# Kernel tuning notes

Measured on AMD Instinct MI355X. Metric: run time of the kernel, lower is better.

The kernel has to match this reference:

```python
import jax, jax.numpy as jnp
import numpy as np

N = 50000      # nodes
E = 800000     # edges (avg degree 16)
LM = 1024      # lm_dim
H = 128        # hidden_channels
OUT = 64       # out_channels


def setup_inputs() -> dict:
    key = jax.random.key(0)
    ks = jax.random.split(key, 13)
    s = 0.02
    return {
        "x": jax.random.normal(ks[0], (N,), dtype=jnp.float32),
        "x_out": jax.random.normal(ks[1], (N, LM), dtype=jnp.float32),
        "c": jax.random.normal(ks[2], (N,), dtype=jnp.float32),
        "edge_index": jax.random.randint(ks[3], (2, E), 0, N, dtype=jnp.int64),
        "edge_weight": jax.random.uniform(ks[4], (E,), dtype=jnp.float32),
        # weights stored as [in, out]
        "Wa": jax.random.normal(ks[5], (1, LM), dtype=jnp.float32) * s,   # aa_linear (no bias)
        "Wc": jax.random.normal(ks[6], (1, LM), dtype=jnp.float32) * s,   # c_linear (no bias)
        "Wl": jax.random.normal(ks[7], (LM, LM), dtype=jnp.float32) * s,  # lm_linear
        "bl": jax.random.normal(ks[8], (LM,), dtype=jnp.float32) * s,
        "W1": jax.random.normal(ks[9], (LM, H), dtype=jnp.float32) * s,   # conv1
        "b1": jax.random.normal(ks[10], (H,), dtype=jnp.float32) * s,
        "W3": jax.random.normal(ks[11], (H, OUT), dtype=jnp.float32) * s,  # conv3
        "b3": jax.random.normal(ks[12], (OUT,), dtype=jnp.float32) * s,
    }


def gcn_conv(h, src, dst, ew, W, b, n):
    """PyG GCNConv with normalize=True, add_self_loops=True."""
    h = h @ W                                   # [n, out]
    loop = jnp.arange(n, dtype=src.dtype)
    src_f = jnp.concatenate([src, loop])
    dst_f = jnp.concatenate([dst, loop])
    ew_f = jnp.concatenate([ew, jnp.ones((n,), ew.dtype)])
    deg = jax.ops.segment_sum(ew_f, dst_f, num_segments=n)     # in-degree incl. self-loops
    dis = jnp.where(deg > 0, jax.lax.rsqrt(deg), 0.0)          # deg^{-1/2}
    norm = dis[src_f] * ew_f * dis[dst_f]                      # per-edge coefficient
    out = jax.ops.segment_sum(norm[:, None] * h[src_f], dst_f, num_segments=n)
    return out + b


def reference(x, x_out, c, edge_index, edge_weight, Wa, Wc, Wl, bl, W1, b1, W3, b3):
    # (c_linear(c[:,None]) + aa_linear(x[:,None]) + lm_linear(x_out)).relu()
    h = jax.nn.relu(c[:, None] * Wc[0] + x[:, None] * Wa[0] + x_out @ Wl + bl)  # [N, LM]
    src, dst = edge_index[0], edge_index[1]
    h = jax.nn.relu(gcn_conv(h, src, dst, edge_weight, W1, b1, N))              # [N, H]
    return gcn_conv(h, src, dst, edge_weight, W3, b3, N)                        # [N, OUT]
```

## Files before the change

### kernel.cpp

```cpp
#include <hip/hip_runtime.h>
#include <hip/hip_bf16.h>

typedef unsigned short u16;
typedef unsigned long long u64;
typedef __attribute__((ext_vector_type(8))) short bf16x8;
typedef __attribute__((ext_vector_type(4))) float f32x4;

constexpr int NN = 50000;
constexpr int NE = 800000;
constexpr int LM = 1024;
constexpr int HC = 128;
constexpr int OC = 64;

constexpr size_t OFF_ROWPTR = 0;
constexpr size_t OFF_CURSOR = 200192;
constexpr size_t OFF_PK     = 400384;
constexpr size_t OFF_INCL   = 800512;
constexpr size_t OFF_BSUM   = 1000704;
constexpr size_t OFF_DIS    = 1000960;
constexpr size_t OFF_META   = 1201152;
constexpr size_t OFF_WLT    = 7601408;
constexpr size_t OFF_W1T    = 9698560;
constexpr size_t OFF_H      = 9960704;
constexpr size_t OFF_Y1     = 112360704;
constexpr size_t OFF_Y3     = 125160704;
constexpr size_t OFF_ABF    = 131560704;
constexpr size_t NEED_FAST  = OFF_ABF + (size_t)NN * LM * 2;

__device__ __forceinline__ u16 f2bf(float f) {
    union { float f; unsigned int u; } a; a.f = f;
    unsigned int u = a.u + 0x7FFFu + ((a.u >> 16) & 1u);
    return (u16)(u >> 16);
}
__device__ __forceinline__ float bf2f(u16 v) {
    union { unsigned int u; float f; } a; a.u = ((unsigned int)v) << 16;
    return a.f;
}
__device__ __forceinline__ ushort2 pkbf(float a, float b) {
    union { __hip_bfloat162 h; ushort2 u; } cv;
    cv.h = __float22bfloat162_rn(make_float2(a, b));
    return cv.u;
}
__device__ __forceinline__ void async_copy16(u16* lds, const u16* g) {
    __builtin_amdgcn_global_load_lds(
        (const __attribute__((address_space(1))) void*)g,
        (__attribute__((address_space(3))) void*)lds, 16, 0, 0);
}

__global__ void k_setup(u64* __restrict__ pk,
                        const float* __restrict__ Wl, u16* __restrict__ WlT,
                        const float* __restrict__ W1, u16* __restrict__ W1T,
                        const float* __restrict__ A32, u16* __restrict__ Abf) {
    int b = blockIdx.x, t = threadIdx.x;
    if (b >= 1732) {
        size_t idx = (size_t)(b - 1732) * 256 + t;
        const float* src = A32 + idx * 8;
        float4 v0 = *(const float4*)(src);
        float4 v1 = *(const float4*)(src + 4);
        union { ushort2 u2[4]; bf16x8 v; } pk2;
        pk2.u2[0] = pkbf(v0.x, v0.y);
        pk2.u2[1] = pkbf(v0.z, v0.w);
        pk2.u2[2] = pkbf(v1.x, v1.y);
        pk2.u2[3] = pkbf(v1.z, v1.w);
        *(bf16x8*)(Abf + idx * 8) = pk2.v;
    } else if (b < 196) {
        int i = b * 256 + t;
        if (i < NN) pk[i] = 0ULL;
    } else if (b < 196 + 1024) {
        __shared__ float sm[32][33];
        int bb = b - 196;
        int n0 = (bb & 31) * 32, k0 = (bb >> 5) * 32;
        int ty = t >> 5, tx = t & 31;
        #pragma unroll
        for (int i = 0; i < 4; i++)
            sm[ty + i * 8][tx] = Wl[(size_t)(k0 + ty + i * 8) * LM + n0 + tx];
        __syncthreads();
        #pragma unroll
        for (int i = 0; i < 4; i++)
            WlT[(size_t)(n0 + ty + i * 8) * LM + k0 + tx] = f2bf(sm[tx][ty + i * 8]);
    } else {
        int idx = (b - 1220) * 256 + t;
        if (idx < HC * LM) {
            int o = idx >> 10, k = idx & 1023;
            W1T[idx] = f2bf(W1[(size_t)k * HC + o]);
        }
    }
}

__global__ void k_count(const int* __restrict__ ei, const float* __restrict__ ew,
                        u64* __restrict__ pk) {
    int e = blockIdx.x * 256 + threadIdx.x;
    if (e < NE) {
        int d = ei[NE + e];
        u64 add = (1ULL << 48) | (u64)(ew[e] * 4294967296.0);
        atomicAdd(&pk[d], add);
    }
}
__global__ void k_scan1(const u64* __restrict__ pk, int* __restrict__ incl,
                        int* __restrict__ bsum) {
    __shared__ int sm[1024];
    int t = threadIdx.x, idx = blockIdx.x * 1024 + t;
    int v = (idx < NN) ? (int)(pk[idx] >> 48) : 0;
    sm[t] = v; __syncthreads();
    for (int off = 1; off < 1024; off <<= 1) {
        int add = (t >= off) ? sm[t - off] : 0;
        __syncthreads();
        sm[t] += add;
        __syncthreads();
    }
    if (idx < NN) incl[idx] = sm[t];
    if (t == 1023) bsum[blockIdx.x] = sm[t];
}
__global__ void k_scan3(const int* __restrict__ incl, const u64* __restrict__ pk,
                        const int* __restrict__ bsum,
                        int* __restrict__ rowptr, int* __restrict__ cursor,
                        float* __restrict__ dis) {
    int seg = blockIdx.x >> 2;
    int lane = threadIdx.x & 63;
    int v = (lane < seg) ? bsum[lane] : 0;
    #pragma unroll
    for (int off = 32; off > 0; off >>= 1) v += __shfl_down(v, off, 64);
    int boffv = __shfl(v, 0, 64);
    int idx = blockIdx.x * 256 + threadIdx.x;
    if (idx < NN) {
        u64 p = pk[idx];
        int cnt = (int)(p >> 48);
        float deg = (float)((double)(p & 0xFFFFFFFFFFFFULL) * 2.3283064365386963e-10);
        int rp = incl[idx] - cnt + boffv;
        rowptr[idx] = rp;
        cursor[idx] = rp;
        dis[idx] = rsqrtf(1.0f + deg);
    } else if (idx == NN) {
        rowptr[NN] = NE;
    }
}
__global__ void k_fill(const int* __restrict__ ei, const float* __restrict__ ew,
                       const float* __restrict__ dis,
                       int* __restrict__ cursor, int2* __restrict__ meta) {
    int e = blockIdx.x * 256 + threadIdx.x;
    if (e < NE) {
        int s = ei[e];
        int d = ei[NE + e];
        int slot = atomicAdd(&cursor[d], 1);
        meta[slot] = make_int2(s, __float_as_int(ew[e] * dis[s]));
    }
}

__global__ __launch_bounds__(256, 4) void k_gemm1a(
    const u16* __restrict__ Abf, const u16* __restrict__ Bt, u16* __restrict__ Cout,
    const float* __restrict__ xv, const float* __restrict__ cv,
    const float* __restrict__ Wa, const float* __restrict__ Wc,
    const float* __restrict__ bl) {
    __shared__ u16 lA[128 * 64];
    __shared__ u16 lB[128 * 64];
    const int tid = threadIdx.x;
    const int lane = tid & 63, wv = tid >> 6;
    int x = blockIdx.x & 7, j = blockIdx.x >> 3;
    int bx = (j & ~7) | x;
    int by = j & 7;
    if (bx >= 391) return;
    const int m0 = bx * 128, n0 = by * 128;
    const int wm = (wv >> 1) * 64, wn = (wv & 1) * 64;
    const int fr = lane & 15, qd = lane >> 4;

    f32x4 acc[4][4] = {};

    for (int kt = 0; kt < 16; kt++) {
        const int k0 = kt << 6;
        __syncthreads();
        #pragma unroll
        for (int i = 0; i < 4; i++) {
            int r0 = i * 32 + wv * 8;
            int rl = r0 + (lane >> 3);
            int slot = lane & 7;
            int k8 = slot ^ (rl & 7);
            const u16* g = Bt + (size_t)(n0 + rl) * LM + k0 + k8 * 8;
            async_copy16(&lB[r0 * 64], g);
        }
        #pragma unroll
        for (int i = 0; i < 4; i++) {
            int r0 = i * 32 + wv * 8;
            int rl = r0 + (lane >> 3);
            int slot = lane & 7;
            int k8 = slot ^ (rl & 7);
            int row = m0 + rl; if (row >= NN) row = NN - 1;
            const u16* g = Abf + (size_t)row * LM + k0 + k8 * 8;
            async_copy16(&lA[r0 * 64], g);
        }
        __syncthreads();
        #pragma unroll
        for (int s = 0; s < 2; s++) {
            const int slot = (s * 4 + qd) ^ (fr & 7);
            bf16x8 af[4], bfm[4];
            #pragma unroll
            for (int mi = 0; mi < 4; mi++)
                af[mi] = *(const bf16x8*)&lA[(wm + mi * 16 + fr) * 64 + slot * 8];
            #pragma unroll
            for (int ni = 0; ni < 4; ni++)
                bfm[ni] = *(const bf16x8*)&lB[(wn + ni * 16 + fr) * 64 + slot * 8];
            #pragma unroll
            for (int mi = 0; mi < 4; mi++)
                #pragma unroll
                for (int ni = 0; ni < 4; ni++)
                    acc[mi][ni] = __builtin_amdgcn_mfma_f32_16x16x32_bf16(
                        af[mi], bfm[ni], acc[mi][ni], 0, 0, 0);
        }
    }

    int jj[4]; float waj[4], wcj[4], blj[4];
    #pragma unroll
    for (int ni = 0; ni < 4; ni++) {
        jj[ni] = n0 + wn + ni * 16 + fr;
        waj[ni] = Wa[jj[ni]]; wcj[ni] = Wc[jj[ni]]; blj[ni] = bl[jj[ni]];
    }
    #pragma unroll
    for (int mi = 0; mi < 4; mi++)
        #pragma unroll
        for (int r = 0; r < 4; r++) {
            int row = m0 + wm + mi * 16 + qd * 4 + r;
            if (row < NN) {
                float xb = xv[row], cb = cv[row];
                #pragma unroll
                for (int ni = 0; ni < 4; ni++) {
                    float v = acc[mi][ni][r] + xb * waj[ni] + cb * wcj[ni] + blj[ni];
                    Cout[(size_t)row * LM + jj[ni]] = f2bf(fmaxf(v, 0.f));
                }
            }
        }
}

__global__ __launch_bounds__(256, 2) void k_gemm1f(
    const float* __restrict__ A32, const u16* __restrict__ Bt, u16* __restrict__ Cout,
    const float* __restrict__ xv, const float* __restrict__ cv,
    const float* __restrict__ Wa, const float* __restrict__ Wc,
    const float* __restrict__ bl) {
    __shared__ u16 lA[128 * 64];
    __shared__ u16 lB[2][128 * 64];
    const int tid = threadIdx.x;
    const int lane = tid & 63, wv = tid >> 6;
    const int bx = ((blockIdx.x >> 5) << 3) | (blockIdx.x & 7);
    const int by = (blockIdx.x >> 3) & 3;
    if (bx >= 391) return;
    const int m0 = bx * 128, n0 = by * 256;
    const int wm = (wv >> 1) * 64, wn = (wv & 1) * 64;
    const int fr = lane & 15, qd = lane >> 4;

    f32x4 acc[2][4][4] = {};

    int srl[4], sslot[4]; const float* sbase[4];
    float4 pf[8];
    #pragma unroll
    for (int i = 0; i < 4; i++) {
        int cidx = i * 256 + tid;
        srl[i] = cidx >> 3; sslot[i] = cidx & 7;
        int k8 = sslot[i] ^ (srl[i] & 7);
        int row = m0 + srl[i]; if (row >= NN) row = NN - 1;
        sbase[i] = A32 + (size_t)row * LM + k8 * 8;
    }
    #pragma unroll
    for (int i = 0; i < 4; i++) {
        pf[2 * i]     = *(const float4*)(sbase[i]);
        pf[2 * i + 1] = *(const float4*)(sbase[i] + 4);
    }

    for (int kt = 0; kt < 16; kt++) {
        const int k0 = kt << 6;
        __syncthreads();
        #pragma unroll
        for (int h = 0; h < 2; h++)
            #pragma unroll
            for (int i = 0; i < 4; i++) {
                int r0 = i * 32 + wv * 8;
                int rl = r0 + (lane >> 3);
                int slot = lane & 7;
                int k8 = slot ^ (rl & 7);
                const u16* g = Bt + (size_t)(n0 + h * 128 + rl) * LM + k0 + k8 * 8;
                async_copy16(&lB[h][r0 * 64], g);
            }
        #pragma unroll
        for (int i = 0; i < 4; i++) {
            union { ushort2 u2[4]; bf16x8 v; } pk;
            pk.u2[0] = pkbf(pf[2 * i].x, pf[2 * i].y);
            pk.u2[1] = pkbf(pf[2 * i].z, pf[2 * i].w);
            pk.u2[2] = pkbf(pf[2 * i + 1].x, pf[2 * i + 1].y);
            pk.u2[3] = pkbf(pf[2 * i + 1].z, pf[2 * i + 1].w);
            *(bf16x8*)&lA[srl[i] * 64 + sslot[i] * 8] = pk.v;
        }
        __syncthreads();
        if (kt < 15) {
            #pragma unroll
            for (int i = 0; i < 4; i++) {
                pf[2 * i]     = *(const float4*)(sbase[i] + k0 + 64);
                pf[2 * i + 1] = *(const float4*)(sbase[i] + k0 + 68);
            }
        }
        #pragma unroll
        for (int s = 0; s < 2; s++) {
            const int slot = (s * 4 + qd) ^ (fr & 7);
            bf16x8 af[4];
            #pragma unroll
            for (int mi = 0; mi < 4; mi++)
                af[mi] = *(const bf16x8*)&lA[(wm + mi * 16 + fr) * 64 + slot * 8];
            #pragma unroll
            for (int h = 0; h < 2; h++) {
                bf16x8 bfm[4];
                #pragma unroll
                for (int ni = 0; ni < 4; ni++)
                    bfm[ni] = *(const bf16x8*)&lB[h][(wn + ni * 16 + fr) * 64 + slot * 8];
                #pragma unroll
                for (int mi = 0; mi < 4; mi++)
                    #pragma unroll
                    for (int ni = 0; ni < 4; ni++)
                        acc[h][mi][ni] = __builtin_amdgcn_mfma_f32_16x16x32_bf16(
                            af[mi], bfm[ni], acc[h][mi][ni], 0, 0, 0);
            }
        }
    }

    #pragma unroll
    for (int h = 0; h < 2; h++) {
        int jj[4]; float waj[4], wcj[4], blj[4];
        #pragma unroll
        for (int ni = 0; ni < 4; ni++) {
            jj[ni] = n0 + h * 128 + wn + ni * 16 + fr;
            waj[ni] = Wa[jj[ni]]; wcj[ni] = Wc[jj[ni]]; blj[ni] = bl[jj[ni]];
        }
        #pragma unroll
        for (int mi = 0; mi < 4; mi++)
            #pragma unroll
            for (int r = 0; r < 4; r++) {
                int row = m0 + wm + mi * 16 + qd * 4 + r;
                if (row < NN) {
                    float xb = xv[row], cb = cv[row];
                    #pragma unroll
                    for (int ni = 0; ni < 4; ni++) {
                        float v = acc[h][mi][ni][r] + xb * waj[ni] + cb * wcj[ni] + blj[ni];
                        Cout[(size_t)row * LM + jj[ni]] = f2bf(fmaxf(v, 0.f));
                    }
                }
            }
    }
}

__global__ __launch_bounds__(256) void k_gemm2(
    const u16* __restrict__ Abf, const u16* __restrict__ Bt, u16* __restrict__ Cout) {
    __shared__ u16 lA[64 * 64];
    __shared__ u16 lB[128 * 64];
    const int tid = threadIdx.x;
    const int lane = tid & 63, wv = tid >> 6;
    const int m0 = blockIdx.x * 64;
    const int wm = (wv >> 1) * 32, wn = (wv & 1) * 64;
    const int fr = lane & 15, qd = lane >> 4;
    f32x4 acc[2][4] = {};

    for (int kt = 0; kt < 16; kt++) {
        const int k0 = kt << 6;
        __syncthreads();
        #pragma unroll
        for (int i = 0; i < 4; i++) {
            int r0 = i * 32 + wv * 8;
            int rl = r0 + (lane >> 3);
            int slot = lane & 7;
            int k8 = slot ^ (rl & 7);
            const u16* g = Bt + (size_t)rl * LM + k0 + k8 * 8;
            async_copy16(&lB[r0 * 64], g);
        }
        #pragma unroll
        for (int i = 0; i < 2; i++) {
            int r0 = i * 32 + wv * 8;
            int rl = r0 + (lane >> 3);
            int slot = lane & 7;
            int k8 = slot ^ (rl & 7);
            int row = m0 + rl; if (row >= NN) row = NN - 1;
            const u16* g = Abf + (size_t)row * LM + k0 + k8 * 8;
            async_copy16(&lA[r0 * 64], g);
        }
        __syncthreads();
        #pragma unroll
        for (int s = 0; s < 2; s++) {
            const int slot = (s * 4 + qd) ^ (fr & 7);
            bf16x8 af[2], bfm[4];
            #pragma unroll
            for (int mi = 0; mi < 2; mi++)
                af[mi] = *(const bf16x8*)&lA[(wm + mi * 16 + fr) * 64 + slot * 8];
            #pragma unroll
            for (int ni = 0; ni < 4; ni++)
                bfm[ni] = *(const bf16x8*)&lB[(wn + ni * 16 + fr) * 64 + slot * 8];
            #pragma unroll
            for (int mi = 0; mi < 2; mi++)
                #pragma unroll
                for (int ni = 0; ni < 4; ni++)
                    acc[mi][ni] = __builtin_amdgcn_mfma_f32_16x16x32_bf16(
                        af[mi], bfm[ni], acc[mi][ni], 0, 0, 0);
        }
    }
    #pragma unroll
    for (int mi = 0; mi < 2; mi++)
        #pragma unroll
        for (int r = 0; r < 4; r++) {
            int row = m0 + wm + mi * 16 + qd * 4 + r;
            if (row < NN) {
                #pragma unroll
                for (int ni = 0; ni < 4; ni++)
                    Cout[(size_t)row * HC + wn + ni * 16 + fr] = f2bf(acc[mi][ni][r]);
            }
        }
}

__global__ __launch_bounds__(512) void k_agg1g3(
    const u16* __restrict__ y1, const int* __restrict__ rowptr,
    const int2* __restrict__ meta, const float* __restrict__ dis,
    const float* __restrict__ b1, const float* __restrict__ W3,
    u16* __restrict__ y3) {
    __shared__ float hrow[8][HC];
    int wv = threadIdx.x >> 6, lane = threadIdx.x & 63;
    int node = blockIdx.x * 8 + wv;
    if (node >= NN) return;
    float di = dis[node];
    int p0 = rowptr[node], p1 = rowptr[node + 1];
    ushort2 sv = *(const ushort2*)(y1 + (size_t)node * HC + lane * 2);
    float a0 = di * bf2f(sv.x), a1 = di * bf2f(sv.y);
    #pragma unroll 8
    for (int p = p0; p < p1; ++p) {
        int2 m = meta[p];
        float nm = __int_as_float(m.y);
        ushort2 v = *(const ushort2*)(y1 + (size_t)m.x * HC + lane * 2);
        a0 += nm * bf2f(v.x);
        a1 += nm * bf2f(v.y);
    }
    a0 = fmaxf(di * a0 + b1[lane * 2], 0.f);
    a1 = fmaxf(di * a1 + b1[lane * 2 + 1], 0.f);
    hrow[wv][lane * 2] = a0;
    hrow[wv][lane * 2 + 1] = a1;
    float acc = 0.f;
    #pragma unroll 8
    for (int k = 0; k < HC; ++k)
        acc += hrow[wv][k] * W3[(size_t)k * OC + lane];
    y3[(size_t)node * OC + lane] = f2bf(acc);
}

__global__ __launch_bounds__(256) void k_agg3(
    const u16* __restrict__ y3, const int* __restrict__ rowptr,
    const int2* __restrict__ meta, const float* __restrict__ dis,
    const float* __restrict__ b3, float* __restrict__ outp) {
    int node = blockIdx.x * 4 + (threadIdx.x >> 6);
    int lane = threadIdx.x & 63;
    if (node >= NN) return;
    float di = dis[node];
    int p0 = rowptr[node], p1 = rowptr[node + 1];
    float a = di * bf2f(y3[(size_t)node * OC + lane]);
    #pragma unroll 8
    for (int p = p0; p < p1; ++p) {
        int2 m = meta[p];
        a += __int_as_float(m.y) * bf2f(y3[(size_t)m.x * OC + lane]);
    }
    outp[(size_t)node * OC + lane] = di * a + b3[lane];
}

extern "C" void kernel_launch(void* const* d_in, const int* in_sizes, int n_in,
                              void* d_out, int out_size, void* d_ws, size_t ws_size,
                              hipStream_t stream) {
    const float* x    = (const float*)d_in[0];
    const float* xout = (const float*)d_in[1];
    const float* c    = (const float*)d_in[2];
    const int*   ei   = (const int*)d_in[3];
    const float* ew   = (const float*)d_in[4];
    const float* Wa   = (const float*)d_in[5];
    const float* Wc   = (const float*)d_in[6];
    const float* Wl   = (const float*)d_in[7];
    const float* bl   = (const float*)d_in[8];
    const float* W1   = (const float*)d_in[9];
    const float* b1   = (const float*)d_in[10];
    const float* W3   = (const float*)d_in[11];
    const float* b3   = (const float*)d_in[12];
    float* outp = (float*)d_out;

    char* ws = (char*)d_ws;
    int*   rowptr = (int*)(ws + OFF_ROWPTR);
    int*   cursor = (int*)(ws + OFF_CURSOR);
    u64*   pk     = (u64*)(ws + OFF_PK);
    int*   incl   = (int*)(ws + OFF_INCL);
    int*   bsum   = (int*)(ws + OFF_BSUM);
    float* dis    = (float*)(ws + OFF_DIS);
    int2*  meta   = (int2*)(ws + OFF_META);
    u16*   WlT    = (u16*)(ws + OFF_WLT);
    u16*   W1T    = (u16*)(ws + OFF_W1T);
    u16*   hbuf   = (u16*)(ws + OFF_H);
    u16*   y1     = (u16*)(ws + OFF_Y1);
    u16*   y3     = (u16*)(ws + OFF_Y3);
    u16*   Abf    = (u16*)(ws + OFF_ABF);

    const bool fast = (ws_size >= NEED_FAST);

    k_setup<<<fast ? 26732 : 1732, 256, 0, stream>>>(pk, Wl, WlT, W1, W1T, xout, Abf);
    k_count<<<3125, 256, 0, stream>>>(ei, ew, pk);
    k_scan1<<<49, 1024, 0, stream>>>(pk, incl, bsum);
    k_scan3<<<196, 256, 0, stream>>>(incl, pk, bsum, rowptr, cursor, dis);
    k_fill <<<3125, 256, 0, stream>>>(ei, ew, dis, cursor, meta);

    if (fast) {
        k_gemm1a<<<392 * 8, 256, 0, stream>>>(Abf, WlT, hbuf, x, c, Wa, Wc, bl);
    } else {
        k_gemm1f<<<49 * 32, 256, 0, stream>>>(xout, WlT, hbuf, x, c, Wa, Wc, bl);
    }
    k_gemm2<<<782, 256, 0, stream>>>(hbuf, W1T, y1);
    k_agg1g3<<<6250, 512, 0, stream>>>(y1, rowptr, meta, dis, b1, W3, y3);
    k_agg3<<<12500, 256, 0, stream>>>(y3, rowptr, meta, dis, b3, outp);
}
```

Measured before the change: 663.7 us.

## Spread x_out bf16 conversion across graph-preprocessing kernels to overlap latency-bound work

```diff
diff --git a/kernel.cpp b/kernel.cpp
--- a/kernel.cpp
+++ b/kernel.cpp
@@ -27,6 +27,12 @@
 constexpr size_t OFF_ABF    = 131560704;
 constexpr size_t NEED_FAST  = OFF_ABF + (size_t)NN * LM * 2;
 
+constexpr size_t CVT_TOTAL = (size_t)NN * LM / 8;
+constexpr size_t CVT_CNT   = 2560000;
+constexpr size_t CVT_SC1   = 1280000;
+constexpr size_t CVT_SC3   = 640000;
+constexpr size_t CVT_FIL   = 1920000;
+
 __device__ __forceinline__ u16 f2bf(float f) {
     union { float f; unsigned int u; } a; a.f = f;
     unsigned int u = a.u + 0x7FFFu + ((a.u >> 16) & 1u);
@@ -46,29 +52,40 @@
         (const __attribute__((address_space(1))) void*)g,
         (__attribute__((address_space(3))) void*)lds, 16, 0, 0);
 }
-
-__global__ void k_setup(u64* __restrict__ pk,
+__device__ __forceinline__ void cvt_chunk(size_t idx, const float* __restrict__ A32,
+                                          u16* __restrict__ Abf) {
+    const float* src = A32 + idx * 8;
+    float4 v0 = *(const float4*)(src);
+    float4 v1 = *(const float4*)(src + 4);
+    union { ushort2 u2[4]; bf16x8 v; } pk2;
+    pk2.u2[0] = pkbf(v0.x, v0.y);
+    pk2.u2[1] = pkbf(v0.z, v0.w);
+    pk2.u2[2] = pkbf(v1.x, v1.y);
+    pk2.u2[3] = pkbf(v1.z, v1.w);
+    *(bf16x8*)(Abf + idx * 8) = pk2.v;
+}
+
+__global__ void k_zero(u64* __restrict__ pk) {
+    int i = blockIdx.x * 256 + threadIdx.x;
+    if (i < NN) pk[i] = 0ULL;
+}
+
+__global__ void k_count(const int* __restrict__ ei, const float* __restrict__ ew,
+                        u64* __restrict__ pk,
                         const float* __restrict__ Wl, u16* __restrict__ WlT,
                         const float* __restrict__ W1, u16* __restrict__ W1T,
                         const float* __restrict__ A32, u16* __restrict__ Abf) {
     int b = blockIdx.x, t = threadIdx.x;
-    if (b >= 1732) {
-        size_t idx = (size_t)(b - 1732) * 256 + t;
-        const float* src = A32 + idx * 8;
-        float4 v0 = *(const float4*)(src);
-        float4 v1 = *(const float4*)(src + 4);
-        union { ushort2 u2[4]; bf16x8 v; } pk2;
-        pk2.u2[0] = pkbf(v0.x, v0.y);
-        pk2.u2[1] = pkbf(v0.z, v0.w);
-        pk2.u2[2] = pkbf(v1.x, v1.y);
-        pk2.u2[3] = pkbf(v1.z, v1.w);
-        *(bf16x8*)(Abf + idx * 8) = pk2.v;
-    } else if (b < 196) {
-        int i = b * 256 + t;
-        if (i < NN) pk[i] = 0ULL;
-    } else if (b < 196 + 1024) {
+    if (b < 3125) {
+        int e = b * 256 + t;
+        if (e < NE) {
+            int d = ei[NE + e];
+            u64 add = (1ULL << 48) | (u64)(ew[e] * 4294967296.0);
+            atomicAdd(&pk[d], add);
+        }
+    } else if (b < 4149) {
         __shared__ float sm[32][33];
-        int bb = b - 196;
+        int bb = b - 3125;
         int n0 = (bb & 31) * 32, k0 = (bb >> 5) * 32;
         int ty = t >> 5, tx = t & 31;
         #pragma unroll
@@ -78,28 +95,27 @@
         #pragma unroll
         for (int i = 0; i < 4; i++)
             WlT[(size_t)(n0 + ty + i * 8) * LM + k0 + tx] = f2bf(sm[tx][ty + i * 8]);
-    } else {
-        int idx = (b - 1220) * 256 + t;
+    } else if (b < 4661) {
+        int idx = (b - 4149) * 256 + t;
         if (idx < HC * LM) {
             int o = idx >> 10, k = idx & 1023;
             W1T[idx] = f2bf(W1[(size_t)k * HC + o]);
         }
-    }
-}
-
-__global__ void k_count(const int* __restrict__ ei, const float* __restrict__ ew,
-                        u64* __restrict__ pk) {
-    int e = blockIdx.x * 256 + threadIdx.x;
-    if (e < NE) {
-        int d = ei[NE + e];
-        u64 add = (1ULL << 48) | (u64)(ew[e] * 4294967296.0);
-        atomicAdd(&pk[d], add);
-    }
-}
+    } else {
+        cvt_chunk((size_t)(b - 4661) * 256 + t, A32, Abf);
+    }
+}
+
 __global__ void k_scan1(const u64* __restrict__ pk, int* __restrict__ incl,
-                        int* __restrict__ bsum) {
+                        int* __restrict__ bsum,
+                        const float* __restrict__ A32, u16* __restrict__ Abf) {
+    int b = blockIdx.x, t = threadIdx.x;
+    if (b >= 49) {
+        cvt_chunk(CVT_CNT + (size_t)(b - 49) * 1024 + t, A32, Abf);
+        return;
+    }
     __shared__ int sm[1024];
-    int t = threadIdx.x, idx = blockIdx.x * 1024 + t;
+    int idx = b * 1024 + t;
     int v = (idx < NN) ? (int)(pk[idx] >> 48) : 0;
     sm[t] = v; __syncthreads();
     for (int off = 1; off < 1024; off <<= 1) {
@@ -109,19 +125,26 @@
         __syncthreads();
     }
     if (idx < NN) incl[idx] = sm[t];
-    if (t == 1023) bsum[blockIdx.x] = sm[t];
-}
+    if (t == 1023) bsum[b] = sm[t];
+}
+
 __global__ void k_scan3(const int* __restrict__ incl, const u64* __restrict__ pk,
                         const int* __restrict__ bsum,
                         int* __restrict__ rowptr, int* __restrict__ cursor,
-                        float* __restrict__ dis) {
-    int seg = blockIdx.x >> 2;
+                        float* __restrict__ dis,
+                        const float* __restrict__ A32, u16* __restrict__ Abf) {
+    int b = blockIdx.x;
+    if (b >= 196) {
+        cvt_chunk(CVT_CNT + CVT_SC1 + (size_t)(b - 196) * 256 + threadIdx.x, A32, Abf);
+        return;
+    }
+    int seg = b >> 2;
     int lane = threadIdx.x & 63;
     int v = (lane < seg) ? bsum[lane] : 0;
     #pragma unroll
     for (int off = 32; off > 0; off >>= 1) v += __shfl_down(v, off, 64);
     int boffv = __shfl(v, 0, 64);
-    int idx = blockIdx.x * 256 + threadIdx.x;
+    int idx = b * 256 + threadIdx.x;
     if (idx < NN) {
         u64 p = pk[idx];
         int cnt = (int)(p >> 48);
@@ -134,10 +157,18 @@
         rowptr[NN] = NE;
     }
 }
+
 __global__ void k_fill(const int* __restrict__ ei, const float* __restrict__ ew,
                        const float* __restrict__ dis,
-                       int* __restrict__ cursor, int2* __restrict__ meta) {
-    int e = blockIdx.x * 256 + threadIdx.x;
+                       int* __restrict__ cursor, int2* __restrict__ meta,
+                       const float* __restrict__ A32, u16* __restrict__ Abf) {
+    int b = blockIdx.x;
+    if (b >= 3125) {
+        cvt_chunk(CVT_CNT + CVT_SC1 + CVT_SC3 + (size_t)(b - 3125) * 256 + threadIdx.x,
+                  A32, Abf);
+        return;
+    }
+    int e = b * 256 + threadIdx.x;
     if (e < NE) {
         int s = ei[e];
         int d = ei[NE + e];
@@ -146,7 +177,7 @@
     }
 }
 
-__global__ __launch_bounds__(256, 4) void k_gemm1a(
+__global__ __launch_bounds__(256, 2) void k_gemm1a(
     const u16* __restrict__ Abf, const u16* __restrict__ Bt, u16* __restrict__ Cout,
     const float* __restrict__ xv, const float* __restrict__ cv,
     const float* __restrict__ Wa, const float* __restrict__ Wc,
@@ -492,11 +523,14 @@
 
     const bool fast = (ws_size >= NEED_FAST);
 
-    k_setup<<<fast ? 26732 : 1732, 256, 0, stream>>>(pk, Wl, WlT, W1, W1T, xout, Abf);
-    k_count<<<3125, 256, 0, stream>>>(ei, ew, pk);
-    k_scan1<<<49, 1024, 0, stream>>>(pk, incl, bsum);
-    k_scan3<<<196, 256, 0, stream>>>(incl, pk, bsum, rowptr, cursor, dis);
-    k_fill <<<3125, 256, 0, stream>>>(ei, ew, dis, cursor, meta);
+    k_zero<<<196, 256, 0, stream>>>(pk);
+    k_count<<<fast ? 14661 : 4661, 256, 0, stream>>>(ei, ew, pk, Wl, WlT, W1, W1T,
+                                                     xout, Abf);
+    k_scan1<<<fast ? 1299 : 49, 1024, 0, stream>>>(pk, incl, bsum, xout, Abf);
+    k_scan3<<<fast ? 2696 : 196, 256, 0, stream>>>(incl, pk, bsum, rowptr, cursor,
+                                                   dis, xout, Abf);
+    k_fill <<<fast ? 10625 : 3125, 256, 0, stream>>>(ei, ew, dis, cursor, meta,
+                                                     xout, Abf);
 
     if (fast) {
         k_gemm1a<<<392 * 8, 256, 0, stream>>>(Abf, WlT, hbuf, x, c, Wa, Wc, bl);
```

Result: faster. 647.5 us (-2.4%).
